# Optimization experiments

Measured on AMD Instinct MI355X. Metric: run time of the kernel, lower is better.

Reference implementation:

```python
import jax, jax.numpy as jnp
import numpy as np

B, SQ, SKV, H, NH = 2, 2048, 2048, 1024, 16
HD = H // NH  # head dim = 64


def setup_inputs() -> dict:
    key = jax.random.key(0)
    ks = jax.random.split(key, 10)
    s = 1.0 / np.sqrt(H)
    return {
        "query_states": jax.random.normal(ks[0], (B, SQ, H), jnp.float32),
        "key_value_states": jax.random.normal(ks[1], (B, SKV, H), jnp.float32),
        "attention_mask": jnp.ones((B, SQ, SKV), jnp.float32),
        "Wq": jax.random.normal(ks[2], (H, H), jnp.float32) * s,
        "bq": jnp.zeros((H,), jnp.float32),
        "Wk": jax.random.normal(ks[3], (H, H), jnp.float32) * s,
        "Wv": jax.random.normal(ks[4], (H, H), jnp.float32) * s,
        "bv": jnp.zeros((H,), jnp.float32),
        "Wo": jax.random.normal(ks[5], (H, H), jnp.float32) * s,
        "bo": jnp.zeros((H,), jnp.float32),
    }


def reference(query_states, key_value_states, attention_mask, Wq, bq, Wk, Wv, bv, Wo, bo):
    # projections (torch Linear: x @ W.T + b; key proj has NO bias)
    q = query_states @ Wq.T + bq            # [B,SQ,H]
    k = key_value_states @ Wk.T              # [B,SKV,H]
    v = key_value_states @ Wv.T + bv         # [B,SKV,H]
    # split heads -> [B, NH, S, HD]
    q = q.reshape(B, SQ, NH, HD).transpose(0, 2, 1, 3)
    k = k.reshape(B, SKV, NH, HD).transpose(0, 2, 1, 3)
    v = v.reshape(B, SKV, NH, HD).transpose(0, 2, 1, 3)
    scale = 1.0 / np.sqrt(HD)
    scores = jnp.einsum("bhqd,bhkd->bhqk", q * scale, k)
    # additive mask: (1 - mask) * -10000, broadcast over heads
    scores = scores + ((1.0 - attention_mask) * -10000.0)[:, None, :, :]
    probs = jax.nn.softmax(scores, axis=-1)  # dropout p=0 (eval) -> identity
    ctx = jnp.einsum("bhqk,bhkd->bhqd", probs, v)
    ctx = ctx.transpose(0, 2, 1, 3).reshape(B, SQ, H)
    return ctx @ Wo.T + bo
```

## Files before the change

kernel.cpp:

```cpp
#include <hip/hip_runtime.h>

typedef unsigned short u16;
typedef unsigned int u32;
typedef short s16x8 __attribute__((ext_vector_type(8)));
typedef float f32x4 __attribute__((ext_vector_type(4)));

#define AS1 __attribute__((address_space(1)))
#define AS3 __attribute__((address_space(3)))


__device__ __forceinline__ u16 f2bf(float f) {
  unsigned u = __float_as_uint(f);
  u += 0x7fffu + ((u >> 16) & 1u);
  return (u16)(u >> 16);
}
__device__ __forceinline__ float bf2f(u16 b) {
  return __uint_as_float(((unsigned)b) << 16);
}
__device__ __forceinline__ u32 pack2(float a, float b) {
  return (u32)f2bf(a) | ((u32)f2bf(b) << 16);
}
__device__ __forceinline__ void gld16(const void* g, void* l) {
  __builtin_amdgcn_global_load_lds((const AS1 unsigned int*)g,
                                   (AS3 unsigned int*)l, 16, 0, 0);
}

__global__ __launch_bounds__(256) void prep_kernel(
    const float* __restrict__ qs, const float* __restrict__ kvs, const float* __restrict__ mk,
    const float* __restrict__ wq, const float* __restrict__ wk, const float* __restrict__ wv,
    const float* __restrict__ wo,
    u16* __restrict__ q_bf, u16* __restrict__ kv_bf, u16* __restrict__ am_bf,
    u16* __restrict__ wq_bf, u16* __restrict__ wk_bf, u16* __restrict__ wv_bf,
    u16* __restrict__ wo_bf)
{
  const int stride = gridDim.x * blockDim.x;
  for (int v = blockIdx.x * blockDim.x + threadIdx.x; v < 5242880; v += stride) {
    const float* s; u16* d; int off; bool ismask = false;
    if (v < 1048576)      { s = qs;  d = q_bf;  off = v; }
    else if (v < 2097152) { s = kvs; d = kv_bf; off = v - 1048576; }
    else if (v < 2359296) { s = wq;  d = wq_bf; off = v - 2097152; }
    else if (v < 2621440) { s = wk;  d = wk_bf; off = v - 2359296; }
    else if (v < 2883584) { s = wv;  d = wv_bf; off = v - 2621440; }
    else if (v < 3145728) { s = wo;  d = wo_bf; off = v - 2883584; }
    else                  { s = mk;  d = am_bf; off = v - 3145728; ismask = true; }
    float4 f = ((const float4*)s)[off];
    if (ismask) {
      f.x = (1.f - f.x) * -10000.f; f.y = (1.f - f.y) * -10000.f;
      f.z = (1.f - f.z) * -10000.f; f.w = (1.f - f.w) * -10000.f;
    }
    ushort4 o;
    o.x = f2bf(f.x); o.y = f2bf(f.y); o.z = f2bf(f.z); o.w = f2bf(f.w);
    ((ushort4*)d)[off] = o;
  }
}

template<int EPI>
__device__ __forceinline__ void gemm_body(
    const u16* __restrict__ A, const u16* __restrict__ W, const float* __restrict__ bias,
    void* __restrict__ outp, float alpha, int m0, int n0)
{
  __shared__ u16 As[3][4096], Bs[3][4096];
  const int tid = threadIdx.x, wave = tid >> 6, lane = tid & 63;
  const int l15 = lane & 15, l4 = lane >> 4;
  const int wr = wave >> 1, wc = wave & 1;

  const int srow = wave * 16 + (lane >> 2);
  const int sslot = ((lane & 3) ^ ((lane >> 3) & 3)) * 8;
  const u16* aS0 = A + (size_t)(m0 + srow) * 1024 + sslot;
  const u16* aS1 = A + (size_t)(m0 + 64 + srow) * 1024 + sslot;
  const u16* bS0 = W + (size_t)(n0 + srow) * 1024 + sslot;
  const u16* bS1 = W + (size_t)(n0 + 64 + srow) * 1024 + sslot;
  const int dOff0 = wave * 512, dOff1 = 2048 + wave * 512;

  const int fswz = ((l15 >> 1) & 3);
  const int afBase = (wr * 64 + l15) * 32 + ((l4 ^ fswz) * 8);
  const int bfBase = (wc * 64 + l15) * 32 + ((l4 ^ fswz) * 8);

  f32x4 acc[4][4] = {};

  auto stage = [&](int buf, int kt) {
    const int ko = kt * 32;
    gld16(aS0 + ko, &As[buf][dOff0]);
    gld16(aS1 + ko, &As[buf][dOff1]);
    gld16(bS0 + ko, &Bs[buf][dOff0]);
    gld16(bS1 + ko, &Bs[buf][dOff1]);
  };

  stage(0, 0);
  stage(1, 1);

  int cb = 0;
  for (int kt = 0; kt < 32; ++kt) {
    if (kt < 31) asm volatile("s_waitcnt vmcnt(4)");
    else         asm volatile("s_waitcnt vmcnt(0)");
    __syncthreads();
    s16x8 af[4], bf[4];
    #pragma unroll
    for (int m = 0; m < 4; ++m) af[m] = *(const s16x8*)&As[cb][afBase + m * 512];
    #pragma unroll
    for (int n = 0; n < 4; ++n) bf[n] = *(const s16x8*)&Bs[cb][bfBase + n * 512];
    if (kt < 30) {
      int sb = cb + 2; if (sb >= 3) sb -= 3;
      stage(sb, kt + 2);
    }
    #pragma unroll
    for (int m = 0; m < 4; ++m)
      #pragma unroll
      for (int n = 0; n < 4; ++n)
        acc[m][n] = __builtin_amdgcn_mfma_f32_16x16x32_bf16(af[m], bf[n], acc[m][n], 0, 0, 0);
    cb = (cb + 1 == 3) ? 0 : cb + 1;
  }

  #pragma unroll
  for (int n = 0; n < 4; ++n) {
    const int col = n0 + wc * 64 + n * 16 + l15;
    #pragma unroll
    for (int m = 0; m < 4; ++m) {
      #pragma unroll
      for (int r = 0; r < 4; ++r) {
        const int row = m0 + wr * 64 + m * 16 + l4 * 4 + r;
        if constexpr (EPI == 0) {
          const float val = (acc[m][n][r] + (bias ? bias[col] : 0.f)) * alpha;
          const int bb = row >> 11, ss = row & 2047, hh = col >> 6, dd = col & 63;
          ((u16*)outp)[(((size_t)(bb * 16 + hh)) * 2048 + ss) * 64 + dd] = f2bf(val);
        } else if constexpr (EPI == 1) {
          ((float*)outp)[(size_t)row * 1024 + col] = acc[m][n][r] + (bias ? bias[col] : 0.f);
        } else {
          const float val = acc[m][n][r] + bias[row];
          const int hh = row >> 6, dd = row & 63, bb = col >> 11, ss = col & 2047;
          ((u16*)outp)[(((size_t)(bb * 16 + hh)) * 64 + dd) * 2048 + ss] = f2bf(val);
        }
      }
    }
  }
}

__global__ __launch_bounds__(256) void gemm_qkv(
    const u16* __restrict__ qbf, const u16* __restrict__ kvbf,
    const u16* __restrict__ wqb, const u16* __restrict__ wkb, const u16* __restrict__ wvb,
    const float* __restrict__ bq, const float* __restrict__ bv,
    u16* __restrict__ Qh, u16* __restrict__ Kh, u16* __restrict__ Vt)
{
  const int bid = blockIdx.x;
  const int swz = (bid & 7) * 32 + (bid >> 3);
  const int which = blockIdx.y;
  if (which == 0)
    gemm_body<0>(qbf, wqb, bq, Qh, 0.125f, (swz >> 3) * 128, (swz & 7) * 128);
  else if (which == 1)
    gemm_body<0>(kvbf, wkb, nullptr, Kh, 1.0f, (swz >> 3) * 128, (swz & 7) * 128);
  else
    gemm_body<2>(wvb, kvbf, bv, Vt, 1.0f, (swz >> 5) * 128, (swz & 31) * 128);
}

__global__ __launch_bounds__(256) void gemm_out(
    const u16* __restrict__ ctx, const u16* __restrict__ wob,
    const float* __restrict__ bo, float* __restrict__ out)
{
  const int bid = blockIdx.x;
  const int swz = (bid & 7) * 32 + (bid >> 3);
  gemm_body<1>(ctx, wob, bo, out, 1.0f, (swz >> 3) * 128, (swz & 7) * 128);
}

__global__ __launch_bounds__(256) void attn_kernel(
    const u16* __restrict__ Qh, const u16* __restrict__ Kh,
    const u16* __restrict__ Vt, const u16* __restrict__ am,
    u16* __restrict__ ctx)
{
  __shared__ u16 Ks[2][4096];
  __shared__ u16 Vs[2][4096];
  __shared__ u16 Pl[4][2][1024];
  const int tid = threadIdx.x, wave = tid >> 6, lane = tid & 63;
  const int l15 = lane & 15, l4 = lane >> 4;
  const int x7 = l15 & 7;
  const int bid = blockIdx.x;
  const int pos = (bid & 7) * 64 + (bid >> 3);
  const int hh = pos >> 4, qt = pos & 15;
  const int b = hh >> 4, h = hh & 15;
  const int q0 = qt * 128;
  const u16* Qb = Qh + (size_t)hh * 2048 * 64;
  const u16* Kb = Kh + (size_t)hh * 2048 * 64;
  const u16* Vb = Vt + (size_t)hh * 64 * 2048;

  s16x8 qf[2][2];
  const u16* amrow[2];
  #pragma unroll
  for (int g = 0; g < 2; ++g) {
    const int qrow = q0 + wave * 32 + g * 16 + l15;
    qf[g][0] = *(const s16x8*)(Qb + (size_t)qrow * 64 + l4 * 8);
    qf[g][1] = *(const s16x8*)(Qb + (size_t)qrow * 64 + 32 + l4 * 8);
    amrow[g] = am + ((size_t)b * 2048 + qrow) * 2048;
  }

  const int sr = wave * 16 + (lane >> 3);
  const int ss = ((lane & 7) ^ ((lane >> 3) & 7)) * 8;
  const u16* kS0 = Kb + (size_t)sr * 64 + ss;
  const u16* kS1 = Kb + (size_t)(sr + 8) * 64 + ss;
  const u16* vS0 = Vb + (size_t)sr * 2048 + ss;
  const u16* vS1 = Vb + (size_t)(sr + 8) * 2048 + ss;
  const int kd0 = wave * 1024, kd1 = kd0 + 512;

  auto stage = [&](int buf, int kt) {
    const int kv0 = kt * 64;
    gld16(kS0 + (size_t)kv0 * 64, &Ks[buf][kd0]);
    gld16(kS1 + (size_t)kv0 * 64, &Ks[buf][kd1]);
    gld16(vS0 + kv0, &Vs[buf][kd0]);
    gld16(vS1 + kv0, &Vs[buf][kd1]);
  };

  f32x4 of[2][4] = {};
  float m_run[2] = {-1e30f, -1e30f}, l_run[2] = {0.f, 0.f};

  stage(0, 0);
  asm volatile("s_waitcnt vmcnt(0)");
  __syncthreads();

  int cur = 0;
  for (int kt = 0; kt < 32; ++kt) {
    if (kt < 31) stage(cur ^ 1, kt + 1);
    const int kv0 = kt * 64;

    ushort4 mk[2][4];
    #pragma unroll
    for (int g = 0; g < 2; ++g)
      #pragma unroll
      for (int nf = 0; nf < 4; ++nf)
        mk[g][nf] = *(const ushort4*)(amrow[g] + kv0 + nf * 16 + l4 * 4);

    f32x4 sf[2][4];
    __builtin_amdgcn_s_setprio(1);
    #pragma unroll
    for (int nf = 0; nf < 4; ++nf) {
      const s16x8 ka0 = *(const s16x8*)&Ks[cur][nf * 1024 + l15 * 64 + ((l4 ^ x7) * 8)];
      const s16x8 ka1 = *(const s16x8*)&Ks[cur][nf * 1024 + l15 * 64 + (((4 + l4) ^ x7) * 8)];
      #pragma unroll
      for (int g = 0; g < 2; ++g) {
        f32x4 s = {0.f, 0.f, 0.f, 0.f};
        s = __builtin_amdgcn_mfma_f32_16x16x32_bf16(ka0, qf[g][0], s, 0, 0, 0);
        s = __builtin_amdgcn_mfma_f32_16x16x32_bf16(ka1, qf[g][1], s, 0, 0, 0);
        sf[g][nf] = s;
      }
    }
    __builtin_amdgcn_s_setprio(0);

    #pragma unroll
    for (int g = 0; g < 2; ++g) {
      float tmax = -1e30f;
      #pragma unroll
      for (int nf = 0; nf < 4; ++nf)
        #pragma unroll
        for (int r = 0; r < 4; ++r) {
          const float sv = sf[g][nf][r] + bf2f(((const u16*)&mk[g][nf])[r]);
          sf[g][nf][r] = sv;
          tmax = fmaxf(tmax, sv);
        }
      tmax = fmaxf(tmax, __shfl_xor(tmax, 16));
      tmax = fmaxf(tmax, __shfl_xor(tmax, 32));

      const float mn = fmaxf(m_run[g], tmax);
      const float sc = __expf(m_run[g] - mn);
      m_run[g] = mn;
      float psum = 0.f;
      u32* pw = (u32*)&Pl[wave][g][0];
      #pragma unroll
      for (int nf = 0; nf < 4; ++nf) {
        const float p0 = __expf(sf[g][nf][0] - mn), p1 = __expf(sf[g][nf][1] - mn);
        const float p2 = __expf(sf[g][nf][2] - mn), p3 = __expf(sf[g][nf][3] - mn);
        psum += (p0 + p1) + (p2 + p3);
        u32* w = pw + l15 * 32 + (((nf * 2 + (l4 >> 1)) ^ x7) * 4) + (l4 & 1) * 2;
        w[0] = pack2(p0, p1);
        w[1] = pack2(p2, p3);
      }
      psum += __shfl_xor(psum, 16);
      psum += __shfl_xor(psum, 32);
      l_run[g] = l_run[g] * sc + psum;

      float sq[4];
      #pragma unroll
      for (int r = 0; r < 4; ++r) sq[r] = __shfl(sc, l4 * 4 + r);
      #pragma unroll
      for (int nd = 0; nd < 4; ++nd)
        #pragma unroll
        for (int r = 0; r < 4; ++r) of[g][nd][r] *= sq[r];
    }

    __builtin_amdgcn_s_setprio(1);
    #pragma unroll
    for (int kh = 0; kh < 2; ++kh) {
      s16x8 pa[2];
      #pragma unroll
      for (int g = 0; g < 2; ++g)
        pa[g] = *(const s16x8*)&Pl[wave][g][l15 * 64 + (((kh * 4 + l4) ^ x7) * 8)];
      #pragma unroll
      for (int nd = 0; nd < 4; ++nd) {
        const s16x8 vb = *(const s16x8*)&Vs[cur][nd * 1024 + l15 * 64 + (((kh * 4 + l4) ^ x7) * 8)];
        #pragma unroll
        for (int g = 0; g < 2; ++g)
          of[g][nd] = __builtin_amdgcn_mfma_f32_16x16x32_bf16(pa[g], vb, of[g][nd], 0, 0, 0);
      }
    }
    __builtin_amdgcn_s_setprio(0);

    asm volatile("s_waitcnt vmcnt(0)");
    __syncthreads();
    cur ^= 1;
  }

  #pragma unroll
  for (int g = 0; g < 2; ++g) {
    const float inv = 1.f / l_run[g];
    float invq[4];
    #pragma unroll
    for (int r = 0; r < 4; ++r) invq[r] = __shfl(inv, l4 * 4 + r);
    #pragma unroll
    for (int r = 0; r < 4; ++r) {
      const int qg = q0 + wave * 32 + g * 16 + l4 * 4 + r;
      const size_t rowbase = ((size_t)b * 2048 + qg) * 1024 + h * 64;
      #pragma unroll
      for (int nd = 0; nd < 4; ++nd)
        ctx[rowbase + nd * 16 + l15] = f2bf(of[g][nd][r] * invq[r]);
    }
  }
}

extern "C" void kernel_launch(void* const* d_in, const int* in_sizes, int n_in,
                              void* d_out, int out_size, void* d_ws, size_t ws_size,
                              hipStream_t stream)
{
  const float* qs = (const float*)d_in[0];
  const float* kvs = (const float*)d_in[1];
  const float* mk = (const float*)d_in[2];
  const float* Wq = (const float*)d_in[3];
  const float* bq = (const float*)d_in[4];
  const float* Wk = (const float*)d_in[5];
  const float* Wv = (const float*)d_in[6];
  const float* bv = (const float*)d_in[7];
  const float* Wo = (const float*)d_in[8];
  const float* bo = (const float*)d_in[9];
  float* out = (float*)d_out;

  char* ws = (char*)d_ws;
  u16* q_bf  = (u16*)(ws + 0);
  u16* kv_bf = (u16*)(ws + 8388608);
  u16* wq_bf = (u16*)(ws + 16777216);
  u16* wk_bf = (u16*)(ws + 18874368);
  u16* wv_bf = (u16*)(ws + 20971520);
  u16* wo_bf = (u16*)(ws + 23068672);
  u16* am_bf = (u16*)(ws + 25165824);
  u16* Qhp   = (u16*)(ws + 41943040);
  u16* Khp   = (u16*)(ws + 50331648);
  u16* Vtp   = (u16*)(ws + 58720256);
  u16* ctxp  = (u16*)(ws + 67108864);

  prep_kernel<<<dim3(2048), dim3(256), 0, stream>>>(
      qs, kvs, mk, Wq, Wk, Wv, Wo, q_bf, kv_bf, am_bf, wq_bf, wk_bf, wv_bf, wo_bf);

  gemm_qkv<<<dim3(256, 3), dim3(256), 0, stream>>>(
      q_bf, kv_bf, wq_bf, wk_bf, wv_bf, bq, bv, Qhp, Khp, Vtp);

  attn_kernel<<<dim3(512), dim3(256), 0, stream>>>(Qhp, Khp, Vtp, am_bf, ctxp);

  gemm_out<<<dim3(256), dim3(256), 0, stream>>>(ctxp, wo_bf, bo, out);
}
```

Measured before the change: 315.3 us.

## Triple-buffer attention K/V, prefetch mask, use exp2 with lazy rescaling

Result: slower. 333.3 us (+5.7%).

```diff
diff --git a/kernel.cpp b/kernel.cpp
--- a/kernel.cpp
+++ b/kernel.cpp
@@ -8,6 +8,7 @@
 #define AS1 __attribute__((address_space(1)))
 #define AS3 __attribute__((address_space(3)))
 
+#define LOG2E 1.4426950408889634f
 
 __device__ __forceinline__ u16 f2bf(float f) {
   unsigned u = __float_as_uint(f);
@@ -24,6 +25,7 @@
   __builtin_amdgcn_global_load_lds((const AS1 unsigned int*)g,
                                    (AS3 unsigned int*)l, 16, 0, 0);
 }
+#define FENCE() asm volatile("" ::: "memory")
 
 __global__ __launch_bounds__(256) void prep_kernel(
     const float* __restrict__ qs, const float* __restrict__ kvs, const float* __restrict__ mk,
@@ -34,6 +36,7 @@
     u16* __restrict__ wo_bf)
 {
   const int stride = gridDim.x * blockDim.x;
+  const float mscale = -10000.f * LOG2E;
   for (int v = blockIdx.x * blockDim.x + threadIdx.x; v < 5242880; v += stride) {
     const float* s; u16* d; int off; bool ismask = false;
     if (v < 1048576)      { s = qs;  d = q_bf;  off = v; }
@@ -45,8 +48,8 @@
     else                  { s = mk;  d = am_bf; off = v - 3145728; ismask = true; }
     float4 f = ((const float4*)s)[off];
     if (ismask) {
-      f.x = (1.f - f.x) * -10000.f; f.y = (1.f - f.y) * -10000.f;
-      f.z = (1.f - f.z) * -10000.f; f.w = (1.f - f.w) * -10000.f;
+      f.x = (1.f - f.x) * mscale; f.y = (1.f - f.y) * mscale;
+      f.z = (1.f - f.z) * mscale; f.w = (1.f - f.w) * mscale;
     }
     ushort4 o;
     o.x = f2bf(f.x); o.y = f2bf(f.y); o.z = f2bf(f.z); o.w = f2bf(f.w);
@@ -91,23 +94,27 @@
 
   int cb = 0;
   for (int kt = 0; kt < 32; ++kt) {
-    if (kt < 31) asm volatile("s_waitcnt vmcnt(4)");
-    else         asm volatile("s_waitcnt vmcnt(0)");
-    __syncthreads();
-    s16x8 af[4], bf[4];
-    #pragma unroll
-    for (int m = 0; m < 4; ++m) af[m] = *(const s16x8*)&As[cb][afBase + m * 512];
-    #pragma unroll
-    for (int n = 0; n < 4; ++n) bf[n] = *(const s16x8*)&Bs[cb][bfBase + n * 512];
+    if (kt < 31) asm volatile("s_waitcnt vmcnt(4)" ::: "memory");
+    else         asm volatile("s_waitcnt vmcnt(0)" ::: "memory");
+    __builtin_amdgcn_s_barrier();
+    FENCE();
     if (kt < 30) {
       int sb = cb + 2; if (sb >= 3) sb -= 3;
       stage(sb, kt + 2);
     }
+    s16x8 af[4], bf[4];
+    #pragma unroll
+    for (int m = 0; m < 4; ++m) af[m] = *(const s16x8*)&As[cb][afBase + m * 512];
+    #pragma unroll
+    for (int n = 0; n < 4; ++n) bf[n] = *(const s16x8*)&Bs[cb][bfBase + n * 512];
+    __builtin_amdgcn_s_setprio(1);
     #pragma unroll
     for (int m = 0; m < 4; ++m)
       #pragma unroll
       for (int n = 0; n < 4; ++n)
         acc[m][n] = __builtin_amdgcn_mfma_f32_16x16x32_bf16(af[m], bf[n], acc[m][n], 0, 0, 0);
+    __builtin_amdgcn_s_setprio(0);
+    FENCE();
     cb = (cb + 1 == 3) ? 0 : cb + 1;
   }
 
@@ -145,7 +152,7 @@
   const int swz = (bid & 7) * 32 + (bid >> 3);
   const int which = blockIdx.y;
   if (which == 0)
-    gemm_body<0>(qbf, wqb, bq, Qh, 0.125f, (swz >> 3) * 128, (swz & 7) * 128);
+    gemm_body<0>(qbf, wqb, bq, Qh, 0.125f * LOG2E, (swz >> 3) * 128, (swz & 7) * 128);
   else if (which == 1)
     gemm_body<0>(kvbf, wkb, nullptr, Kh, 1.0f, (swz >> 3) * 128, (swz & 7) * 128);
   else
@@ -166,8 +173,8 @@
     const u16* __restrict__ Vt, const u16* __restrict__ am,
     u16* __restrict__ ctx)
 {
-  __shared__ u16 Ks[2][4096];
-  __shared__ u16 Vs[2][4096];
+  __shared__ u16 Ks[3][4096];
+  __shared__ u16 Vs[3][4096];
   __shared__ u16 Pl[4][2][1024];
   const int tid = threadIdx.x, wave = tid >> 6, lane = tid & 63;
   const int l15 = lane & 15, l4 = lane >> 4;
@@ -209,22 +216,33 @@
 
   f32x4 of[2][4] = {};
   float m_run[2] = {-1e30f, -1e30f}, l_run[2] = {0.f, 0.f};
+  ushort4 mkC[2][4], mkN[2][4];
 
   stage(0, 0);
-  asm volatile("s_waitcnt vmcnt(0)");
-  __syncthreads();
+  stage(1, 1);
+  #pragma unroll
+  for (int g = 0; g < 2; ++g)
+    #pragma unroll
+    for (int nf = 0; nf < 4; ++nf)
+      mkC[g][nf] = *(const ushort4*)(amrow[g] + nf * 16 + l4 * 4);
+  asm volatile("s_waitcnt vmcnt(0)" ::: "memory");
+  __builtin_amdgcn_s_barrier();
+  FENCE();
 
   int cur = 0;
   for (int kt = 0; kt < 32; ++kt) {
-    if (kt < 31) stage(cur ^ 1, kt + 1);
-    const int kv0 = kt * 64;
-
-    ushort4 mk[2][4];
-    #pragma unroll
-    for (int g = 0; g < 2; ++g)
-      #pragma unroll
-      for (int nf = 0; nf < 4; ++nf)
-        mk[g][nf] = *(const ushort4*)(amrow[g] + kv0 + nf * 16 + l4 * 4);
+    if (kt < 31) {
+      const int kvn = (kt + 1) * 64;
+      #pragma unroll
+      for (int g = 0; g < 2; ++g)
+        #pragma unroll
+        for (int nf = 0; nf < 4; ++nf)
+          mkN[g][nf] = *(const ushort4*)(amrow[g] + kvn + nf * 16 + l4 * 4);
+    }
+    if (kt < 30) {
+      int sb = cur + 2; if (sb >= 3) sb -= 3;
+      stage(sb, kt + 2);
+    }
 
     f32x4 sf[2][4];
     __builtin_amdgcn_s_setprio(1);
@@ -249,22 +267,35 @@
       for (int nf = 0; nf < 4; ++nf)
         #pragma unroll
         for (int r = 0; r < 4; ++r) {
-          const float sv = sf[g][nf][r] + bf2f(((const u16*)&mk[g][nf])[r]);
+          const float sv = sf[g][nf][r] + bf2f(((const u16*)&mkC[g][nf])[r]);
           sf[g][nf][r] = sv;
           tmax = fmaxf(tmax, sv);
         }
       tmax = fmaxf(tmax, __shfl_xor(tmax, 16));
       tmax = fmaxf(tmax, __shfl_xor(tmax, 32));
 
-      const float mn = fmaxf(m_run[g], tmax);
-      const float sc = __expf(m_run[g] - mn);
-      m_run[g] = mn;
+      const float mOld = m_run[g];
+      float mn = mOld;
+      if (!__all(tmax <= mOld + 11.54f)) {
+        mn = fmaxf(mOld, tmax);
+        const float sc = exp2f(mOld - mn);
+        m_run[g] = mn;
+        l_run[g] *= sc;
+        float sq[4];
+        #pragma unroll
+        for (int r = 0; r < 4; ++r) sq[r] = __shfl(sc, l4 * 4 + r);
+        #pragma unroll
+        for (int nd = 0; nd < 4; ++nd)
+          #pragma unroll
+          for (int r = 0; r < 4; ++r) of[g][nd][r] *= sq[r];
+      }
+
       float psum = 0.f;
       u32* pw = (u32*)&Pl[wave][g][0];
       #pragma unroll
       for (int nf = 0; nf < 4; ++nf) {
-        const float p0 = __expf(sf[g][nf][0] - mn), p1 = __expf(sf[g][nf][1] - mn);
-        const float p2 = __expf(sf[g][nf][2] - mn), p3 = __expf(sf[g][nf][3] - mn);
+        const float p0 = exp2f(sf[g][nf][0] - mn), p1 = exp2f(sf[g][nf][1] - mn);
+        const float p2 = exp2f(sf[g][nf][2] - mn), p3 = exp2f(sf[g][nf][3] - mn);
         psum += (p0 + p1) + (p2 + p3);
         u32* w = pw + l15 * 32 + (((nf * 2 + (l4 >> 1)) ^ x7) * 4) + (l4 & 1) * 2;
         w[0] = pack2(p0, p1);
@@ -272,15 +303,7 @@
       }
       psum += __shfl_xor(psum, 16);
       psum += __shfl_xor(psum, 32);
-      l_run[g] = l_run[g] * sc + psum;
-
-      float sq[4];
-      #pragma unroll
-      for (int r = 0; r < 4; ++r) sq[r] = __shfl(sc, l4 * 4 + r);
-      #pragma unroll
-      for (int nd = 0; nd < 4; ++nd)
-        #pragma unroll
-        for (int r = 0; r < 4; ++r) of[g][nd][r] *= sq[r];
+      l_run[g] += psum;
     }
 
     __builtin_amdgcn_s_setprio(1);
@@ -300,9 +323,18 @@
     }
     __builtin_amdgcn_s_setprio(0);
 
-    asm volatile("s_waitcnt vmcnt(0)");
-    __syncthreads();
-    cur ^= 1;
+    #pragma unroll
+    for (int g = 0; g < 2; ++g)
+      #pragma unroll
+      for (int nf = 0; nf < 4; ++nf)
+        mkC[g][nf] = mkN[g][nf];
+
+    if (kt < 31) {
+      asm volatile("s_waitcnt vmcnt(4)" ::: "memory");
+      __builtin_amdgcn_s_barrier();
+      FENCE();
+    }
+    cur = (cur + 1 == 3) ? 0 : cur + 1;
   }
 
   #pragma unroll
```
